# Kernel tuning notes

Hardware: AMD Instinct MI355X
Metric: run time of the kernel (lower is better)

## Reference

```python
import jax, jax.numpy as jnp
import numpy as np
import math

B, S, D, H = 2, 2048, 1024, 16
HS = D // H  # head_size = 64


def setup_inputs() -> dict:
    key = jax.random.key(0)
    ks = jax.random.split(key, 5)
    scale = 0.02
    return {
        "q": jax.random.normal(ks[0], (B, S, D), dtype=jnp.float32),
        "Wq": jax.random.normal(ks[1], (D, D), dtype=jnp.float32) * scale,
        "bq": jnp.zeros((D,), dtype=jnp.float32),
        "Wk": jax.random.normal(ks[2], (D, D), dtype=jnp.float32) * scale,
        "bk": jnp.zeros((D,), dtype=jnp.float32),
        "Wv": jax.random.normal(ks[3], (D, D), dtype=jnp.float32) * scale,
        "bv": jnp.zeros((D,), dtype=jnp.float32),
        "Wo": jax.random.normal(ks[4], (D, D), dtype=jnp.float32) * scale,
        "bo": jnp.zeros((D,), dtype=jnp.float32),
    }


def reference(q, Wq, bq, Wk, bk, Wv, bv, Wo, bo) -> jnp.ndarray:
    # self-attention: k = v = q (source defaults), is_causal=True, dropout=0 (eval)
    b, s, d = q.shape
    qh = (q @ Wq + bq).reshape(b, s, H, HS).transpose(0, 2, 1, 3)  # [B,H,S,HS]
    kh = (q @ Wk + bk).reshape(b, s, H, HS).transpose(0, 2, 1, 3)
    vh = (q @ Wv + bv).reshape(b, s, H, HS).transpose(0, 2, 1, 3)
    scores = jnp.einsum("bhqd,bhkd->bhqk", qh, kh) / math.sqrt(HS)  # [B,H,S,S]
    causal = jnp.triu(jnp.ones((s, s), dtype=bool), k=1)
    scores = jnp.where(causal, -jnp.inf, scores)
    attn = jax.nn.softmax(scores, axis=-1)
    out = jnp.einsum("bhqk,bhkd->bhqd", attn, vh)  # [B,H,S,HS]
    out = out.transpose(0, 2, 1, 3).reshape(b, s, d)
    return out @ Wo + bo
```

## Files before the change

### kernel.cpp

```cpp
#include <hip/hip_runtime.h>
#include <hip/hip_bf16.h>

typedef unsigned short u16;
typedef __attribute__((ext_vector_type(8))) __bf16 bf16x8;
typedef __attribute__((ext_vector_type(4))) float f32x4;

#define S_LEN 2048
#define DMODEL 1024
#define NHEAD 16
#define HSZ 64

__device__ __forceinline__ u16 f2bf(float f) {
  union { __hip_bfloat16 b; u16 u; } c;
  c.b = __float2bfloat16(f);
  return c.u;
}

__device__ __forceinline__ float bf2f(u16 u) {
  union { unsigned int i; float f; } c;
  c.i = ((unsigned int)u) << 16;
  return c.f;
}

__device__ __forceinline__ float fexp2(float x) {
#if __has_builtin(__builtin_amdgcn_exp2f)
  return __builtin_amdgcn_exp2f(x);
#else
  return exp2f(x);
#endif
}

__device__ __forceinline__ unsigned int cvtpk(float lo, float hi) {
  unsigned int r;
  asm("v_cvt_pk_bf16_f32 %0, %1, %2" : "=v"(r) : "v"(lo), "v"(hi));
  return r;
}

__device__ __forceinline__ void gload_lds16(const void* g, void* l) {
  __builtin_amdgcn_global_load_lds(
      (const __attribute__((address_space(1))) void*)g,
      (__attribute__((address_space(3))) void*)l, 16, 0, 0);
}

__device__ __forceinline__ f32x4 mfma16(bf16x8 a, bf16x8 b, f32x4 c) {
  return __builtin_amdgcn_mfma_f32_16x16x32_bf16(a, b, c, 0, 0, 0);
}

__global__ __launch_bounds__(256) void convert_f2b_kernel(const float* __restrict__ in,
                                                          u16* __restrict__ out) {
  int i = (blockIdx.x * 256 + threadIdx.x) * 4;
  float4 v = *(const float4*)(in + i);
  ushort4 o;
  o.x = f2bf(v.x); o.y = f2bf(v.y); o.z = f2bf(v.z); o.w = f2bf(v.w);
  *(ushort4*)(out + i) = o;
}

__global__ __launch_bounds__(256) void transpose_w_kernel(
    const float* __restrict__ W0, const float* __restrict__ W1,
    const float* __restrict__ W2, const float* __restrict__ W3,
    u16* __restrict__ T0, u16* __restrict__ T1,
    u16* __restrict__ T2, u16* __restrict__ T3) {
  int z = blockIdx.z;
  const float* W = (z == 0) ? W0 : ((z == 1) ? W1 : ((z == 2) ? W2 : W3));
  u16* T = (z == 0) ? T0 : ((z == 1) ? T1 : ((z == 2) ? T2 : T3));
  __shared__ float tile[64][65];
  int t = threadIdx.x;
  int k0 = blockIdx.y * 64, n0 = blockIdx.x * 64;
#pragma unroll
  for (int j = 0; j < 4; ++j) {
    int idx = j * 256 + t;
    int row = idx >> 4, c4 = idx & 15;
    float4 v = *(const float4*)(W + (size_t)(k0 + row) * DMODEL + n0 + c4 * 4);
    tile[row][c4 * 4 + 0] = v.x; tile[row][c4 * 4 + 1] = v.y;
    tile[row][c4 * 4 + 2] = v.z; tile[row][c4 * 4 + 3] = v.w;
  }
  __syncthreads();
#pragma unroll
  for (int j = 0; j < 4; ++j) {
    int idx = j * 256 + t;
    int orow = idx >> 4, c4 = idx & 15;
    ushort4 o;
    o.x = f2bf(tile[c4 * 4 + 0][orow]);
    o.y = f2bf(tile[c4 * 4 + 1][orow]);
    o.z = f2bf(tile[c4 * 4 + 2][orow]);
    o.w = f2bf(tile[c4 * 4 + 3][orow]);
    *(ushort4*)(T + (size_t)(n0 + orow) * DMODEL + k0 + c4 * 4) = o;
  }
}

__global__ __launch_bounds__(256) void transpose_v_kernel(const u16* __restrict__ Vh,
                                                          u16* __restrict__ Vt) {
  int bh = blockIdx.y;
  int s0 = blockIdx.x * 64;
  __shared__ __align__(16) u16 tile[64][72];
  int t = threadIdx.x;
#pragma unroll
  for (int j = 0; j < 4; ++j) {
    int idx = j * 256 + t;
    int row = idx >> 4, c4 = idx & 15;
    *(ushort4*)&tile[row][c4 * 4] =
        *(const ushort4*)(Vh + ((size_t)bh * S_LEN + s0 + row) * HSZ + c4 * 4);
  }
  __syncthreads();
#pragma unroll
  for (int j = 0; j < 4; ++j) {
    int idx = j * 256 + t;
    int orow = idx >> 4, c4 = idx & 15;
    ushort4 o;
    o.x = tile[c4 * 4 + 0][orow];
    o.y = tile[c4 * 4 + 1][orow];
    o.z = tile[c4 * 4 + 2][orow];
    o.w = tile[c4 * 4 + 3][orow];
    *(ushort4*)(Vt + ((size_t)bh * HSZ + orow) * S_LEN + s0 + c4 * 4) = o;
  }
}

template <int WM>
__device__ __forceinline__ void gemm_core(const u16* __restrict__ A,
                                          const u16* __restrict__ Bt,
                                          u16* ldsbuf, f32x4 (&acc)[WM][4],
                                          int m0, int n0) {
  const int t = threadIdx.x;
  const int wave = t >> 6, lane = t & 63;
  const int l15 = lane & 15, l4 = lane >> 4;
  const int wr = wave >> 1, wc = wave & 1;
  u16* Asm = ldsbuf;
  u16* Bsm = ldsbuf + WM * 1024;
  for (int kt = 0; kt < DMODEL / 32; ++kt) {
    int kb = kt * 32;
#pragma unroll
    for (int j = 0; j < WM / 2; ++j) {
      int ci = j * 256 + t;
      int row = ci >> 2, kc = ci & 3;
      gload_lds16(A + (size_t)(m0 + row) * DMODEL + kb + kc * 8,
                  Asm + (j * 256 + wave * 64) * 8);
    }
#pragma unroll
    for (int j = 0; j < 2; ++j) {
      int ci = j * 256 + t;
      int row = ci >> 2, kc = ci & 3;
      gload_lds16(Bt + (size_t)(n0 + row) * DMODEL + kb + kc * 8,
                  Bsm + (j * 256 + wave * 64) * 8);
    }
    __syncthreads();
    bf16x8 af[WM], bfr[4];
#pragma unroll
    for (int m = 0; m < WM; ++m)
      af[m] = *(const bf16x8*)(Asm + ((wr * (WM * 16) + m * 16 + l15) * 32 + l4 * 8));
#pragma unroll
    for (int n = 0; n < 4; ++n)
      bfr[n] = *(const bf16x8*)(Bsm + ((wc * 64 + n * 16 + l15) * 32 + l4 * 8));
#pragma unroll
    for (int m = 0; m < WM; ++m)
#pragma unroll
      for (int n = 0; n < 4; ++n)
        acc[m][n] = mfma16(af[m], bfr[n], acc[m][n]);
    __syncthreads();
  }
}

__global__ __launch_bounds__(256) void gemm_qkv_kernel(
    const u16* __restrict__ A, const u16* __restrict__ B0, const u16* __restrict__ B1,
    const u16* __restrict__ B2, const float* __restrict__ bias0,
    const float* __restrict__ bias1, const float* __restrict__ bias2,
    u16* __restrict__ d0, u16* __restrict__ d1, u16* __restrict__ d2) {
  __shared__ __align__(16) u16 lds[8192];
  int z = blockIdx.z;
  const u16* Bt = (z == 0) ? B0 : ((z == 1) ? B1 : B2);
  const float* bias = (z == 0) ? bias0 : ((z == 1) ? bias1 : bias2);
  u16* dst = (z == 0) ? d0 : ((z == 1) ? d1 : d2);
  const float sc = (z == 0) ? 0.18033688011112042f : 1.0f;
  int m0 = blockIdx.y * 128, n0 = blockIdx.x * 128;
  f32x4 acc[4][4] = {};
  gemm_core<4>(A, Bt, lds, acc, m0, n0);
  const int t = threadIdx.x;
  const int wave = t >> 6, lane = t & 63, l15 = lane & 15, l4 = lane >> 4;
  const int wr = wave >> 1, wc = wave & 1;
#pragma unroll
  for (int n = 0; n < 4; ++n) {
    int colg = n0 + wc * 64 + n * 16 + l15;
    float bn = bias[colg];
    int h = colg >> 6, hs = colg & 63;
#pragma unroll
    for (int m = 0; m < 4; ++m) {
#pragma unroll
      for (int i = 0; i < 4; ++i) {
        int rowg = m0 + wr * 64 + m * 16 + 4 * l4 + i;
        int b = rowg >> 11, s = rowg & 2047;
        dst[(size_t)(b * NHEAD + h) * S_LEN * HSZ + (size_t)s * HSZ + hs] =
            f2bf((acc[m][n][i] + bn) * sc);
      }
    }
  }
}

__global__ __launch_bounds__(256) void gemm_out_kernel(const u16* __restrict__ A,
                                                       const u16* __restrict__ Bt,
                                                       const float* __restrict__ bias,
                                                       float* __restrict__ out) {
  __shared__ __align__(16) u16 lds[6144];
  int m0 = blockIdx.y * 64, n0 = blockIdx.x * 128;
  f32x4 acc[2][4] = {};
  gemm_core<2>(A, Bt, lds, acc, m0, n0);
  const int t = threadIdx.x;
  const int wave = t >> 6, lane = t & 63, l15 = lane & 15, l4 = lane >> 4;
  const int wr = wave >> 1, wc = wave & 1;
#pragma unroll
  for (int n = 0; n < 4; ++n) {
    int colg = n0 + wc * 64 + n * 16 + l15;
    float bn = bias[colg];
#pragma unroll
    for (int m = 0; m < 2; ++m) {
#pragma unroll
      for (int i = 0; i < 4; ++i) {
        int rowg = m0 + wr * 32 + m * 16 + 4 * l4 + i;
        out[(size_t)rowg * DMODEL + colg] = acc[m][n][i] + bn;
      }
    }
  }
}

__global__ __launch_bounds__(512, 2) void attn_kernel(const u16* __restrict__ Qh,
                                                      const u16* __restrict__ Kh,
                                                      const u16* __restrict__ Vt,
                                                      u16* __restrict__ Ob) {
  __shared__ __align__(16) u16 Ksm[64][72];
  __shared__ __align__(16) u16 Vsm[64][72];
  __shared__ __align__(16) u16 Pl[8][16][72];
  const int tixd = threadIdx.x;
  const int wave = tixd >> 6, lane = tixd & 63;
  const int l15 = lane & 15, l4 = lane >> 4;
  const int id = blockIdx.x;
  const int bh = (id & 7) * 4 + ((id >> 3) & 3);
  const int pk = id >> 5;
  const u16* Qb = Qh + (size_t)bh * S_LEN * HSZ;
  const u16* Kb = Kh + (size_t)bh * S_LEN * HSZ;
  const u16* Vb = Vt + (size_t)bh * HSZ * S_LEN;
  const int shbase = l4 * 20;
  u16 (*P)[72] = Pl[wave];
  const int b = bh >> 4, h = bh & 15;
  const int sr = tixd >> 3;
  const int sc = (tixd & 7) * 8;

#pragma unroll 1
  for (int ph = 0; ph < 2; ++ph) {
    const int pp = ph ? (15 - pk) : pk;
    const int q0 = pp * 128 + wave * 16;
    const int nt = 2 * pp + 2;

    bf16x8 qf[2];
#pragma unroll
    for (int kc = 0; kc < 2; ++kc)
      qf[kc] = *(const bf16x8*)(Qb + (size_t)(q0 + l15) * HSZ + kc * 32 + l4 * 8);

    f32x4 oacc[4] = {};
    float mrun = -1e30f;
    float lrun = 0.f;

    uint4 ka = *(const uint4*)(Kb + (size_t)sr * HSZ + sc);
    uint4 va = *(const uint4*)(Vb + (size_t)sr * S_LEN + sc);

#pragma unroll 1
    for (int t = 0; t < nt; ++t) {
      __syncthreads();
      *(uint4*)&Ksm[sr][sc] = ka;
      *(uint4*)&Vsm[sr][sc] = va;
      __syncthreads();
      if (t + 1 < nt) {
        const int kvn = (t + 1) * 64;
        ka = *(const uint4*)(Kb + (size_t)(kvn + sr) * HSZ + sc);
        va = *(const uint4*)(Vb + (size_t)sr * S_LEN + kvn + sc);
      }
      const int kv0 = t * 64;

      bf16x8 kf[4][2];
#pragma unroll
      for (int n = 0; n < 4; ++n)
#pragma unroll
        for (int kc = 0; kc < 2; ++kc)
          kf[n][kc] = *(const bf16x8*)&Ksm[n * 16 + l15][kc * 32 + l4 * 8];

      f32x4 sacc[4] = {};
#pragma unroll
      for (int n = 0; n < 4; ++n) {
        sacc[n] = mfma16(kf[n][0], qf[0], sacc[n]);
        sacc[n] = mfma16(kf[n][1], qf[1], sacc[n]);
      }

      bf16x8 vf[2][4];
#pragma unroll
      for (int kb = 0; kb < 2; ++kb)
#pragma unroll
        for (int n = 0; n < 4; ++n)
          vf[kb][n] = *(const bf16x8*)&Vsm[n * 16 + l15][kb * 32 + l4 * 8];

      if (kv0 + 63 > q0) {
#pragma unroll
        for (int n = 0; n < 4; ++n)
#pragma unroll
          for (int i = 0; i < 4; ++i)
            if (kv0 + n * 16 + 4 * l4 + i > q0 + l15) sacc[n][i] = -1e30f;
      }

      {
        float a0 = fmaxf(fmaxf(sacc[0][0], sacc[0][1]),
                         fmaxf(sacc[0][2], sacc[0][3]));
        float a1 = fmaxf(fmaxf(sacc[1][0], sacc[1][1]),
                         fmaxf(sacc[1][2], sacc[1][3]));
        float a2 = fmaxf(fmaxf(sacc[2][0], sacc[2][1]),
                         fmaxf(sacc[2][2], sacc[2][3]));
        float a3 = fmaxf(fmaxf(sacc[3][0], sacc[3][1]),
                         fmaxf(sacc[3][2], sacc[3][3]));
        float tm = fmaxf(fmaxf(a0, a1), fmaxf(a2, a3));
        tm = fmaxf(tm, __shfl_xor(tm, 16));
        tm = fmaxf(tm, __shfl_xor(tm, 32));
        float mnew = fmaxf(mrun, tm);
        float corr = fexp2(mrun - mnew);
        mrun = mnew;
        float rs = 0.f;
#pragma unroll
        for (int n = 0; n < 4; ++n)
#pragma unroll
          for (int i = 0; i < 4; ++i) {
            float pv = fexp2(sacc[n][i] - mnew);
            sacc[n][i] = pv;
            rs += pv;
          }
        rs += __shfl_xor(rs, 16);
        rs += __shfl_xor(rs, 32);
        lrun = lrun * corr + rs;
        float cc0 = __shfl(corr, shbase + 0);
        float cc1 = __shfl(corr, shbase + 1);
        float cc2 = __shfl(corr, shbase + 2);
        float cc3 = __shfl(corr, shbase + 3);
#pragma unroll
        for (int n = 0; n < 4; ++n) {
          oacc[n][0] *= cc0; oacc[n][1] *= cc1;
          oacc[n][2] *= cc2; oacc[n][3] *= cc3;
        }
#pragma unroll
        for (int n = 0; n < 4; ++n) {
          uint2 pkk;
          pkk.x = cvtpk(sacc[n][0], sacc[n][1]);
          pkk.y = cvtpk(sacc[n][2], sacc[n][3]);
          *(uint2*)&P[l15][n * 16 + 4 * l4] = pkk;
        }
      }

#pragma unroll
      for (int kb = 0; kb < 2; ++kb) {
        bf16x8 pf = *(const bf16x8*)&P[l15][kb * 32 + l4 * 8];
#pragma unroll
        for (int n = 0; n < 4; ++n)
          oacc[n] = mfma16(pf, vf[kb][n], oacc[n]);
      }
    }

    {
      float invm = 1.0f / lrun;
#pragma unroll
      for (int i = 0; i < 4; ++i) {
        float iv = __shfl(invm, shbase + i);
        int srow = q0 + 4 * l4 + i;
#pragma unroll
        for (int n = 0; n < 4; ++n) {
          int d = h * HSZ + n * 16 + l15;
          Ob[((size_t)b * S_LEN + srow) * DMODEL + d] = f2bf(oacc[n][i] * iv);
        }
      }
    }
  }
}

extern "C" void kernel_launch(void* const* d_in, const int* in_sizes, int n_in,
                              void* d_out, int out_size, void* d_ws, size_t ws_size,
                              hipStream_t stream) {
  const float* q  = (const float*)d_in[0];
  const float* Wq = (const float*)d_in[1];
  const float* bq = (const float*)d_in[2];
  const float* Wk = (const float*)d_in[3];
  const float* bk = (const float*)d_in[4];
  const float* Wv = (const float*)d_in[5];
  const float* bv = (const float*)d_in[6];
  const float* Wo = (const float*)d_in[7];
  const float* bo = (const float*)d_in[8];

  char* ws = (char*)d_ws;
  const size_t MB = 1024 * 1024;
  u16* Xb  = (u16*)(ws + 0);
  u16* WqT = (u16*)(ws + 8 * MB);
  u16* WkT = (u16*)(ws + 10 * MB);
  u16* WvT = (u16*)(ws + 12 * MB);
  u16* WoT = (u16*)(ws + 14 * MB);
  u16* Qh  = (u16*)(ws + 16 * MB);
  u16* Kh  = (u16*)(ws + 24 * MB);
  u16* Vh  = (u16*)(ws + 32 * MB);
  u16* Vt  = (u16*)(ws + 40 * MB);
  u16* Ob  = (u16*)(ws + 48 * MB);

  convert_f2b_kernel<<<4096, 256, 0, stream>>>(q, Xb);
  transpose_w_kernel<<<dim3(16, 16, 4), 256, 0, stream>>>(Wq, Wk, Wv, Wo,
                                                          WqT, WkT, WvT, WoT);
  gemm_qkv_kernel<<<dim3(8, 32, 3), 256, 0, stream>>>(Xb, WqT, WkT, WvT,
                                                      bq, bk, bv, Qh, Kh, Vh);
  transpose_v_kernel<<<dim3(32, 32), 256, 0, stream>>>(Vh, Vt);
  attn_kernel<<<256, 512, 0, stream>>>(Qh, Kh, Vt, Ob);
  gemm_out_kernel<<<dim3(8, 64), 256, 0, stream>>>(Ob, WoT, bo, (float*)d_out);
}
```

Measured before the change: 115.9 us.

## Merge prep kernels, enlarge out-proj tile, double-buffer K/V in attention

Folds the input bf16 conversion and the weight transpose into one prep kernel, which removes a launch. Doubles the output-projection GEMM tile to 128x128, halving the grid and using gemm_core<4>. In attention, K/V shared-memory tiles are double-buffered so each iteration needs one barrier instead of two, and the next tile's register-to-LDS store happens after the compute. This trades more LDS per block and fewer out-GEMM blocks (256 on a large GPU) for less synchronisation and launch overhead.

```diff
diff --git a/kernel.cpp b/kernel.cpp
--- a/kernel.cpp
+++ b/kernel.cpp
@@ -46,26 +46,29 @@
   return __builtin_amdgcn_mfma_f32_16x16x32_bf16(a, b, c, 0, 0, 0);
 }
 
-__global__ __launch_bounds__(256) void convert_f2b_kernel(const float* __restrict__ in,
-                                                          u16* __restrict__ out) {
-  int i = (blockIdx.x * 256 + threadIdx.x) * 4;
-  float4 v = *(const float4*)(in + i);
-  ushort4 o;
-  o.x = f2bf(v.x); o.y = f2bf(v.y); o.z = f2bf(v.z); o.w = f2bf(v.w);
-  *(ushort4*)(out + i) = o;
-}
-
-__global__ __launch_bounds__(256) void transpose_w_kernel(
+__global__ __launch_bounds__(256) void prep_kernel(
+    const float* __restrict__ qin, u16* __restrict__ Xb,
     const float* __restrict__ W0, const float* __restrict__ W1,
     const float* __restrict__ W2, const float* __restrict__ W3,
     u16* __restrict__ T0, u16* __restrict__ T1,
     u16* __restrict__ T2, u16* __restrict__ T3) {
-  int z = blockIdx.z;
+  __shared__ float tile[64][65];
+  int bid = blockIdx.x;
+  int t = threadIdx.x;
+  if (bid < 4096) {
+    int i = (bid * 256 + t) * 4;
+    float4 v = *(const float4*)(qin + i);
+    ushort4 o;
+    o.x = f2bf(v.x); o.y = f2bf(v.y); o.z = f2bf(v.z); o.w = f2bf(v.w);
+    *(ushort4*)(Xb + i) = o;
+    return;
+  }
+  int id = bid - 4096;
+  int z = id >> 8;
+  int r = id & 255;
+  int k0 = (r >> 4) * 64, n0 = (r & 15) * 64;
   const float* W = (z == 0) ? W0 : ((z == 1) ? W1 : ((z == 2) ? W2 : W3));
   u16* T = (z == 0) ? T0 : ((z == 1) ? T1 : ((z == 2) ? T2 : T3));
-  __shared__ float tile[64][65];
-  int t = threadIdx.x;
-  int k0 = blockIdx.y * 64, n0 = blockIdx.x * 64;
 #pragma unroll
   for (int j = 0; j < 4; ++j) {
     int idx = j * 256 + t;
@@ -198,10 +201,10 @@
                                                        const u16* __restrict__ Bt,
                                                        const float* __restrict__ bias,
                                                        float* __restrict__ out) {
-  __shared__ __align__(16) u16 lds[6144];
-  int m0 = blockIdx.y * 64, n0 = blockIdx.x * 128;
-  f32x4 acc[2][4] = {};
-  gemm_core<2>(A, Bt, lds, acc, m0, n0);
+  __shared__ __align__(16) u16 lds[8192];
+  int m0 = blockIdx.y * 128, n0 = blockIdx.x * 128;
+  f32x4 acc[4][4] = {};
+  gemm_core<4>(A, Bt, lds, acc, m0, n0);
   const int t = threadIdx.x;
   const int wave = t >> 6, lane = t & 63, l15 = lane & 15, l4 = lane >> 4;
   const int wr = wave >> 1, wc = wave & 1;
@@ -210,10 +213,10 @@
     int colg = n0 + wc * 64 + n * 16 + l15;
     float bn = bias[colg];
 #pragma unroll
-    for (int m = 0; m < 2; ++m) {
+    for (int m = 0; m < 4; ++m) {
 #pragma unroll
       for (int i = 0; i < 4; ++i) {
-        int rowg = m0 + wr * 32 + m * 16 + 4 * l4 + i;
+        int rowg = m0 + wr * 64 + m * 16 + 4 * l4 + i;
         out[(size_t)rowg * DMODEL + colg] = acc[m][n][i] + bn;
       }
     }
@@ -224,8 +227,8 @@
                                                       const u16* __restrict__ Kh,
                                                       const u16* __restrict__ Vt,
                                                       u16* __restrict__ Ob) {
-  __shared__ __align__(16) u16 Ksm[64][72];
-  __shared__ __align__(16) u16 Vsm[64][72];
+  __shared__ __align__(16) u16 Ksm[2][64][72];
+  __shared__ __align__(16) u16 Vsm[2][64][72];
   __shared__ __align__(16) u16 Pl[8][16][72];
   const int tixd = threadIdx.x;
   const int wave = tixd >> 6, lane = tixd & 63;
@@ -259,18 +262,19 @@
 
     uint4 ka = *(const uint4*)(Kb + (size_t)sr * HSZ + sc);
     uint4 va = *(const uint4*)(Vb + (size_t)sr * S_LEN + sc);
+    __syncthreads();
+    *(uint4*)&Ksm[0][sr][sc] = ka;
+    *(uint4*)&Vsm[0][sr][sc] = va;
 
 #pragma unroll 1
     for (int t = 0; t < nt; ++t) {
-      __syncthreads();
-      *(uint4*)&Ksm[sr][sc] = ka;
-      *(uint4*)&Vsm[sr][sc] = va;
-      __syncthreads();
+      const int cur = t & 1;
       if (t + 1 < nt) {
         const int kvn = (t + 1) * 64;
         ka = *(const uint4*)(Kb + (size_t)(kvn + sr) * HSZ + sc);
         va = *(const uint4*)(Vb + (size_t)sr * S_LEN + kvn + sc);
       }
+      __syncthreads();
       const int kv0 = t * 64;
 
       bf16x8 kf[4][2];
@@ -278,7 +282,7 @@
       for (int n = 0; n < 4; ++n)
 #pragma unroll
         for (int kc = 0; kc < 2; ++kc)
-          kf[n][kc] = *(const bf16x8*)&Ksm[n * 16 + l15][kc * 32 + l4 * 8];
+          kf[n][kc] = *(const bf16x8*)&Ksm[cur][n * 16 + l15][kc * 32 + l4 * 8];
 
       f32x4 sacc[4] = {};
 #pragma unroll
@@ -292,7 +296,7 @@
       for (int kb = 0; kb < 2; ++kb)
 #pragma unroll
         for (int n = 0; n < 4; ++n)
-          vf[kb][n] = *(const bf16x8*)&Vsm[n * 16 + l15][kb * 32 + l4 * 8];
+          vf[kb][n] = *(const bf16x8*)&Vsm[cur][n * 16 + l15][kb * 32 + l4 * 8];
 
       if (kv0 + 63 > q0) {
 #pragma unroll
@@ -354,6 +358,11 @@
         for (int n = 0; n < 4; ++n)
           oacc[n] = mfma16(pf, vf[kb][n], oacc[n]);
       }
+
+      if (t + 1 < nt) {
+        *(uint4*)&Ksm[cur ^ 1][sr][sc] = ka;
+        *(uint4*)&Vsm[cur ^ 1][sr][sc] = va;
+      }
     }
 
     {
@@ -398,12 +407,11 @@
   u16* Vt  = (u16*)(ws + 40 * MB);
   u16* Ob  = (u16*)(ws + 48 * MB);
 
-  convert_f2b_kernel<<<4096, 256, 0, stream>>>(q, Xb);
-  transpose_w_kernel<<<dim3(16, 16, 4), 256, 0, stream>>>(Wq, Wk, Wv, Wo,
-                                                          WqT, WkT, WvT, WoT);
+  prep_kernel<<<5120, 256, 0, stream>>>(q, Xb, Wq, Wk, Wv, Wo,
+                                        WqT, WkT, WvT, WoT);
   gemm_qkv_kernel<<<dim3(8, 32, 3), 256, 0, stream>>>(Xb, WqT, WkT, WvT,
                                                       bq, bk, bv, Qh, Kh, Vh);
   transpose_v_kernel<<<dim3(32, 32), 256, 0, stream>>>(Vh, Vt);
   attn_kernel<<<256, 512, 0, stream>>>(Qh, Kh, Vt, Ob);
-  gemm_out_kernel<<<dim3(8, 64), 256, 0, stream>>>(Ob, WoT, bo, (float*)d_out);
-}
+  gemm_out_kernel<<<dim3(8, 32), 256, 0, stream>>>(Ob, WoT, bo, (float*)d_out);
+}
```

After: 118.4 us. 2.2% more time.
